# Kernel optimization log

Hardware: AMD Instinct MI355X
Metric: run time of the kernel (lower is better)

The kernel has to match this reference:

```python
import jax, jax.numpy as jnp
import numpy as np

B, D_MODEL, C, T = 2, 256, 64, 1024
N_HEADS = 8
EPS = 1e-5


def setup_inputs() -> dict:
    key = jax.random.key(0)
    k1, k2, k3 = jax.random.split(key, 3)
    x = jax.random.normal(k1, (B, D_MODEL, C, T), dtype=jnp.float32)
    in_w = jax.random.normal(k2, (3 * D_MODEL, D_MODEL), dtype=jnp.float32) * 0.05
    in_b = jnp.zeros((3 * D_MODEL,), jnp.float32)
    out_w = jax.random.normal(k3, (D_MODEL, D_MODEL), dtype=jnp.float32) * 0.05
    out_b = jnp.zeros((D_MODEL,), jnp.float32)
    return dict(x=x, in_w=in_w, in_b=in_b, out_w=out_w, out_b=out_b)


def reference(x, in_w, in_b, out_w, out_b):
    b, d, c, t = x.shape
    h = N_HEADS
    f = d // h
    scale = 1.0 / np.sqrt(f).astype(np.float32)

    # InstanceNorm2d (no affine): normalize each (b, channel) over spatial (c, t)
    mu = x.mean(axis=(2, 3), keepdims=True)
    var = x.var(axis=(2, 3), keepdims=True)  # biased, as torch
    xn = (x - mu) / jnp.sqrt(var + EPS)

    # 1x1 conv d -> 3d
    qkv = jnp.einsum('bdct,ed->bect', xn, in_w) + in_b[None, :, None, None]
    q, k, v = jnp.split(qkv, 3, axis=1)

    def to_heads(u):
        # b (h f) c t -> (b c) h f t
        u = u.reshape(b, h, f, c, t)
        u = u.transpose(0, 3, 1, 2, 4)
        return u.reshape(b * c, h, f, t)

    q = jax.nn.softmax(to_heads(q), axis=-2) * scale  # softmax over feature dim
    k = jax.nn.softmax(to_heads(k), axis=-1)          # softmax over length dim
    v = to_heads(v) / t

    # context: [n, h, f_k, f_v]
    ctx = jnp.einsum('nhkl,nhvl->nhkv', k, v)
    out = jnp.einsum('nhdv,nhdl->nhvl', ctx, q)

    # (b c) h f t -> b (h f) c t
    out = out.reshape(b, c, h, f, t).transpose(0, 2, 3, 1, 4).reshape(b, d, c, t)

    out = jnp.einsum('bdct,ed->bect', out, out_w) + out_b[None, :, None, None]
    return out + x
```

## Files before the change

kernel.cpp:

```cpp
#include <hip/hip_runtime.h>
#include <stdint.h>

#define D_MODEL 256
#define TDIM    1024
#define NHEADS  8
#define FDIM    32
#define P_LEN   65536
#define K3      768
#define BK      64

using u16 = unsigned short;

typedef __bf16 bf16x8 __attribute__((ext_vector_type(8)));
typedef float  floatx4 __attribute__((ext_vector_type(4)));

__device__ __forceinline__ float b2f(u16 u) {
    union { float f; uint32_t i; } v; v.i = ((uint32_t)u) << 16; return v.f;
}
__device__ __forceinline__ u16 f2b(float f) {
    union { float f; uint32_t i; } v; v.f = f;
    uint32_t i = v.i;
    uint32_t r = i + 0x7fffu + ((i >> 16) & 1u);
    return (u16)(r >> 16);
}

__device__ __forceinline__ void gload_lds16(const u16* g, u16* l) {
    __builtin_amdgcn_global_load_lds((const __attribute__((address_space(1))) void*)g,
                                     (__attribute__((address_space(3))) void*)l,
                                     16, 0, 0);
}

__device__ __forceinline__ void stc(u16* p, float v) { *p = f2b(v); }
__device__ __forceinline__ void stc(float* p, float v) { *p = v; }

__global__ __launch_bounds__(256) void stats_kernel(const float* __restrict__ x,
                                                    float* __restrict__ mu,
                                                    float* __restrict__ rstd) {
    int bd = blockIdx.x;
    const float* row = x + (size_t)bd * P_LEN;
    int tid = threadIdx.x;
    float s = 0.f, sq = 0.f;
    for (int i = 0; i < P_LEN / (256 * 4); ++i) {
        int idx = (i * 256 + tid) * 4;
        float4 u = *(const float4*)(row + idx);
        s += u.x + u.y + u.z + u.w;
        sq += u.x * u.x + u.y * u.y + u.z * u.z + u.w * u.w;
    }
    for (int off = 32; off; off >>= 1) { s += __shfl_down(s, off); sq += __shfl_down(sq, off); }
    __shared__ float rs[4], rq[4];
    if ((tid & 63) == 0) { rs[tid >> 6] = s; rq[tid >> 6] = sq; }
    __syncthreads();
    if (tid == 0) {
        float S = rs[0] + rs[1] + rs[2] + rs[3];
        float Q = rq[0] + rq[1] + rq[2] + rq[3];
        float m = S * (1.f / 65536.f);
        float var = Q * (1.f / 65536.f) - m * m;
        mu[bd] = m;
        rstd[bd] = rsqrtf(var + 1e-5f);
    }
}

__global__ __launch_bounds__(256) void fold_kernel(const float* __restrict__ in_w,
                                                   const float* __restrict__ in_b,
                                                   const float* __restrict__ mu,
                                                   const float* __restrict__ rstd,
                                                   u16* __restrict__ Wp,
                                                   float* __restrict__ bprime) {
    int bid = blockIdx.x;
    int b = bid / K3, e = bid % K3;
    int d = threadIdx.x;
    float w = in_w[e * D_MODEL + d];
    float r = rstd[b * D_MODEL + d];
    float m = mu[b * D_MODEL + d];
    Wp[(size_t)bid * D_MODEL + d] = f2b(w * r);
    float contrib = w * r * m;
    for (int off = 32; off; off >>= 1) contrib += __shfl_down(contrib, off);
    __shared__ float rr[4];
    if ((d & 63) == 0) rr[d >> 6] = contrib;
    __syncthreads();
    if (d == 0) bprime[bid] = in_b[e] - (rr[0] + rr[1] + rr[2] + rr[3]);
}

__global__ void cvt_w(const float* __restrict__ w, u16* __restrict__ o) {
    int i = blockIdx.x * 256 + threadIdx.x;
    o[i] = f2b(w[i]);
}

__global__ __launch_bounds__(256) void transpose_x(const float* __restrict__ x,
                                                   u16* __restrict__ xt) {
    __shared__ float tile[64][65];
    int p0 = blockIdx.x * 64;
    int d0 = blockIdx.y * 64;
    int tid = threadIdx.x;
    int dr = tid >> 4;
    int pc = (tid & 15) * 4;
#pragma unroll
    for (int it = 0; it < 4; ++it) {
        int d = it * 16 + dr;
        float4 v = *(const float4*)&x[(size_t)(d0 + d) * P_LEN + p0 + pc];
        tile[pc + 0][d] = v.x;
        tile[pc + 1][d] = v.y;
        tile[pc + 2][d] = v.z;
        tile[pc + 3][d] = v.w;
    }
    __syncthreads();
    int pr = tid >> 3;
    int dc = (tid & 7) * 8;
#pragma unroll
    for (int it = 0; it < 2; ++it) {
        int p = it * 32 + pr;
        ushort4 o0 = make_ushort4(f2b(tile[p][dc + 0]), f2b(tile[p][dc + 1]),
                                  f2b(tile[p][dc + 2]), f2b(tile[p][dc + 3]));
        ushort4 o1 = make_ushort4(f2b(tile[p][dc + 4]), f2b(tile[p][dc + 5]),
                                  f2b(tile[p][dc + 6]), f2b(tile[p][dc + 7]));
        u16* dst = xt + (size_t)(p0 + p) * D_MODEL + d0 + dc;
        *(ushort4*)dst = o0;
        *(ushort4*)(dst + 4) = o1;
    }
}

template <bool RESID, typename OT>
__global__ __launch_bounds__(256) void mgemm(const u16* __restrict__ A,
                                             const u16* __restrict__ Bt,
                                             const float* __restrict__ bias,
                                             const float* __restrict__ resid,
                                             OT* __restrict__ Cout) {
    __shared__ __align__(16) u16 As[128 * BK];
    __shared__ __align__(16) u16 Bs[128 * BK];
    const int tid  = threadIdx.x;
    const int wave = tid >> 6;
    const int lane = tid & 63;
    const int m0 = blockIdx.y * 128;
    const int p0 = blockIdx.x * 128;
    const int mw = (wave >> 1) * 64;
    const int nw = (wave & 1) * 64;

    floatx4 acc[4][4];
#pragma unroll
    for (int i = 0; i < 4; ++i)
#pragma unroll
        for (int j = 0; j < 4; ++j) acc[i][j] = (floatx4){0.f, 0.f, 0.f, 0.f};

    const int srow = lane >> 3;
    const int schunk = lane & 7;
    const int q  = lane >> 4;
    const int rl = lane & 15;

    for (int s = 0; s < 4; ++s) {
        const int k0 = s * BK;
#pragma unroll
        for (int j = 0; j < 4; ++j) {
            int rbase = wave * 32 + j * 8;
            int r = rbase + srow;
            int cg = schunk ^ (r & 7);
            gload_lds16(A  + ((size_t)(m0 + r) << 8) + k0 + cg * 8, &As[rbase * BK]);
            gload_lds16(Bt + ((size_t)(p0 + r) << 8) + k0 + cg * 8, &Bs[rbase * BK]);
        }
        __syncthreads();
#pragma unroll
        for (int ks = 0; ks < 2; ++ks) {
            bf16x8 af[4], bf[4];
#pragma unroll
            for (int ti = 0; ti < 4; ++ti) {
                int r = mw + 16 * ti + rl;
                int cp = (ks * 4 + q) ^ (r & 7);
                af[ti] = *(const bf16x8*)&As[r * BK + cp * 8];
            }
#pragma unroll
            for (int tj = 0; tj < 4; ++tj) {
                int r = nw + 16 * tj + rl;
                int cp = (ks * 4 + q) ^ (r & 7);
                bf[tj] = *(const bf16x8*)&Bs[r * BK + cp * 8];
            }
#pragma unroll
            for (int ti = 0; ti < 4; ++ti)
#pragma unroll
                for (int tj = 0; tj < 4; ++tj)
                    acc[ti][tj] = __builtin_amdgcn_mfma_f32_16x16x32_bf16(
                        af[ti], bf[tj], acc[ti][tj], 0, 0, 0);
        }
        __syncthreads();
    }

#pragma unroll
    for (int ti = 0; ti < 4; ++ti) {
#pragma unroll
        for (int i = 0; i < 4; ++i) {
            int e = m0 + mw + 16 * ti + 4 * q + i;
            float bv = bias[e];
            size_t rowbase = (size_t)e * P_LEN + p0 + nw;
#pragma unroll
            for (int tj = 0; tj < 4; ++tj) {
                size_t addr = rowbase + 16 * tj + rl;
                float v = acc[ti][tj][i] + bv;
                if (RESID) v += resid[addr];
                stc(Cout + addr, v);
            }
        }
    }
}

__global__ __launch_bounds__(256) void attn_k(const u16* __restrict__ qkv,
                                              u16* __restrict__ attT) {
    int bid = blockIdx.x;
    int c = bid >> 3, h = bid & 7;
    int tid = threadIdx.x;
    size_t colbase = (size_t)c * TDIM;
    const u16* qb = qkv + (size_t)(h * FDIM) * P_LEN + colbase;
    const u16* kb = qkv + (size_t)(D_MODEL + h * FDIM) * P_LEN + colbase;
    const u16* vb = qkv + (size_t)(2 * D_MODEL + h * FDIM) * P_LEN + colbase;

    __shared__ float kmax[32], kinv[32];
    __shared__ float ekt[32][65];
    __shared__ float vt[64][36];
    __shared__ float ctxs[32][36];

    int row = tid >> 3, g = tid & 7;
    const u16* krow = kb + (size_t)row * P_LEN;

    float m = -1e30f;
    for (int i = 0; i < 32; ++i) {
        ushort4 u = *(const ushort4*)(krow + g * 4 + i * 32);
        m = fmaxf(m, fmaxf(fmaxf(b2f(u.x), b2f(u.y)), fmaxf(b2f(u.z), b2f(u.w))));
    }
    for (int off = 4; off; off >>= 1) m = fmaxf(m, __shfl_down(m, off, 8));
    if (g == 0) kmax[row] = m;
    __syncthreads();
    float rm = kmax[row];
    float s = 0.f;
    for (int i = 0; i < 32; ++i) {
        ushort4 u = *(const ushort4*)(krow + g * 4 + i * 32);
        s += __expf(b2f(u.x) - rm) + __expf(b2f(u.y) - rm) +
             __expf(b2f(u.z) - rm) + __expf(b2f(u.w) - rm);
    }
    for (int off = 4; off; off >>= 1) s += __shfl_down(s, off, 8);
    if (g == 0) kinv[row] = 1.f / (s * (float)TDIM);
    __syncthreads();

    float mymax = kmax[row];
    float myinv = kinv[row];
    const u16* vrow = vb + (size_t)row * P_LEN;

    int kd = tid >> 3, vg = tid & 7;
    float cacc[4] = {0.f, 0.f, 0.f, 0.f};
    for (int tile = 0; tile < 16; ++tile) {
        int t0 = tile * 64;
        int col = g * 8;
        ushort4 u1 = *(const ushort4*)(krow + t0 + col);
        ushort4 u2 = *(const ushort4*)(krow + t0 + col + 4);
        ushort4 w1 = *(const ushort4*)(vrow + t0 + col);
        ushort4 w2 = *(const ushort4*)(vrow + t0 + col + 4);
        __syncthreads();
        ekt[row][col + 0] = __expf(b2f(u1.x) - mymax) * myinv;
        ekt[row][col + 1] = __expf(b2f(u1.y) - mymax) * myinv;
        ekt[row][col + 2] = __expf(b2f(u1.z) - mymax) * myinv;
        ekt[row][col + 3] = __expf(b2f(u1.w) - mymax) * myinv;
        ekt[row][col + 4] = __expf(b2f(u2.x) - mymax) * myinv;
        ekt[row][col + 5] = __expf(b2f(u2.y) - mymax) * myinv;
        ekt[row][col + 6] = __expf(b2f(u2.z) - mymax) * myinv;
        ekt[row][col + 7] = __expf(b2f(u2.w) - mymax) * myinv;
        vt[col + 0][row] = b2f(w1.x);
        vt[col + 1][row] = b2f(w1.y);
        vt[col + 2][row] = b2f(w1.z);
        vt[col + 3][row] = b2f(w1.w);
        vt[col + 4][row] = b2f(w2.x);
        vt[col + 5][row] = b2f(w2.y);
        vt[col + 6][row] = b2f(w2.z);
        vt[col + 7][row] = b2f(w2.w);
        __syncthreads();
#pragma unroll 16
        for (int t = 0; t < 64; ++t) {
            float e = ekt[kd][t];
            float4 v4 = *(const float4*)&vt[t][vg * 4];
            cacc[0] += e * v4.x;
            cacc[1] += e * v4.y;
            cacc[2] += e * v4.z;
            cacc[3] += e * v4.w;
        }
    }
    __syncthreads();
    const float scale = 0.17677669529663687f;
    ctxs[kd][vg * 4 + 0] = cacc[0] * scale;
    ctxs[kd][vg * 4 + 1] = cacc[1] * scale;
    ctxs[kd][vg * 4 + 2] = cacc[2] * scale;
    ctxs[kd][vg * 4 + 3] = cacc[3] * scale;
    __syncthreads();

    for (int pair = 0; pair < 2; ++pair) {
        int t1 = tid + pair * 512;
        int t2 = t1 + 256;
        float pa[32], pb[32];
        float ma = -1e30f, mb = -1e30f;
#pragma unroll
        for (int f = 0; f < 32; ++f) {
            pa[f] = b2f(qb[(size_t)f * P_LEN + t1]);
            pb[f] = b2f(qb[(size_t)f * P_LEN + t2]);
            ma = fmaxf(ma, pa[f]);
            mb = fmaxf(mb, pb[f]);
        }
        float sa = 0.f, sb = 0.f;
#pragma unroll
        for (int f = 0; f < 32; ++f) {
            pa[f] = __expf(pa[f] - ma); sa += pa[f];
            pb[f] = __expf(pb[f] - mb); sb += pb[f];
        }
        float ia = 1.f / sa, ib = 1.f / sb;
#pragma unroll
        for (int f = 0; f < 32; ++f) { pa[f] *= ia; pb[f] *= ib; }

        size_t r1 = (size_t)(colbase + t1) * D_MODEL + h * FDIM;
        size_t r2 = (size_t)(colbase + t2) * D_MODEL + h * FDIM;
        for (int vg2 = 0; vg2 < 8; ++vg2) {
            float4 a1 = {0.f, 0.f, 0.f, 0.f}, a2 = {0.f, 0.f, 0.f, 0.f};
#pragma unroll
            for (int kd2 = 0; kd2 < 32; ++kd2) {
                float4 c4 = *(const float4*)&ctxs[kd2][vg2 * 4];
                a1.x += pa[kd2] * c4.x; a1.y += pa[kd2] * c4.y;
                a1.z += pa[kd2] * c4.z; a1.w += pa[kd2] * c4.w;
                a2.x += pb[kd2] * c4.x; a2.y += pb[kd2] * c4.y;
                a2.z += pb[kd2] * c4.z; a2.w += pb[kd2] * c4.w;
            }
            *(ushort4*)&attT[r1 + vg2 * 4] =
                make_ushort4(f2b(a1.x), f2b(a1.y), f2b(a1.z), f2b(a1.w));
            *(ushort4*)&attT[r2 + vg2 * 4] =
                make_ushort4(f2b(a2.x), f2b(a2.y), f2b(a2.z), f2b(a2.w));
        }
    }
}

extern "C" void kernel_launch(void* const* d_in, const int* in_sizes, int n_in,
                              void* d_out, int out_size, void* d_ws, size_t ws_size,
                              hipStream_t stream) {
    const float* x     = (const float*)d_in[0];
    const float* in_w  = (const float*)d_in[1];
    const float* in_b  = (const float*)d_in[2];
    const float* out_w = (const float*)d_in[3];
    const float* out_b = (const float*)d_in[4];
    float* out = (float*)d_out;

    char* ws = (char*)d_ws;
    float* mu     = (float*)(ws);
    float* rstd   = (float*)(ws + 2048);
    u16*   Wp     = (u16*)(ws + 4096);
    float* bprime = (float*)(ws + 790528);
    u16*   Wp2    = (u16*)(ws + 796672);
    u16*   tbuf   = (u16*)(ws + 927744);
    u16*   qkvb   = (u16*)(ws + 34482176);

    stats_kernel<<<512, 256, 0, stream>>>(x, mu, rstd);
    fold_kernel<<<1536, 256, 0, stream>>>(in_w, in_b, mu, rstd, Wp, bprime);
    cvt_w<<<256, 256, 0, stream>>>(out_w, Wp2);

    for (int b = 0; b < 2; ++b) {
        const float* xb = x + (size_t)b * D_MODEL * P_LEN;
        transpose_x<<<dim3(1024, 4), 256, 0, stream>>>(xb, tbuf);
        mgemm<false, u16><<<dim3(512, 6), 256, 0, stream>>>(
            Wp + (size_t)b * K3 * D_MODEL, tbuf, bprime + b * K3, nullptr, qkvb);
        attn_k<<<512, 256, 0, stream>>>(qkvb, tbuf);
        mgemm<true, float><<<dim3(512, 2), 256, 0, stream>>>(
            Wp2, tbuf, out_b, xb, out + (size_t)b * D_MODEL * P_LEN);
    }
}
```

Baseline: 642.5 us.

## Fold attention context into per-channel output weights and use MFMA for context

Splits the attention kernel in two. One kernel computes the q softmax and writes it in transposed layout. The other computes the k-softmax·vᵀ context with bf16 MFMA on LDS tiles. A new wfold kernel multiplies out_w by each per-c context, producing per-channel folded weights. The output GEMM then reads its A operand per channel block, so the context multiply is absorbed into that GEMM and the scalar per-token context product disappears. The max subtraction in both softmaxes is dropped, which risks exp overflow for large activations. The ctx and folded-weight buffers reuse the q region of the qkv buffer after it has been consumed.

```diff
diff --git a/kernel.cpp b/kernel.cpp
--- a/kernel.cpp
+++ b/kernel.cpp
@@ -17,11 +17,20 @@
 __device__ __forceinline__ float b2f(u16 u) {
     union { float f; uint32_t i; } v; v.i = ((uint32_t)u) << 16; return v.f;
 }
+__device__ __forceinline__ float b2f_lo(uint32_t u) {
+    union { float f; uint32_t i; } v; v.i = u << 16; return v.f;
+}
+__device__ __forceinline__ float b2f_hi(uint32_t u) {
+    union { float f; uint32_t i; } v; v.i = u & 0xffff0000u; return v.f;
+}
 __device__ __forceinline__ u16 f2b(float f) {
     union { float f; uint32_t i; } v; v.f = f;
     uint32_t i = v.i;
     uint32_t r = i + 0x7fffu + ((i >> 16) & 1u);
     return (u16)(r >> 16);
+}
+__device__ __forceinline__ uint32_t pack2(float lo, float hi) {
+    return ((uint32_t)f2b(hi) << 16) | (uint32_t)f2b(lo);
 }
 
 __device__ __forceinline__ void gload_lds16(const u16* g, u16* l) {
@@ -81,11 +90,6 @@
     if (d == 0) bprime[bid] = in_b[e] - (rr[0] + rr[1] + rr[2] + rr[3]);
 }
 
-__global__ void cvt_w(const float* __restrict__ w, u16* __restrict__ o) {
-    int i = blockIdx.x * 256 + threadIdx.x;
-    o[i] = f2b(w[i]);
-}
-
 __global__ __launch_bounds__(256) void transpose_x(const float* __restrict__ x,
                                                    u16* __restrict__ xt) {
     __shared__ float tile[64][65];
@@ -119,7 +123,7 @@
     }
 }
 
-template <bool RESID, typename OT>
+template <bool RESID, bool PERC, typename OT>
 __global__ __launch_bounds__(256) void mgemm(const u16* __restrict__ A,
                                              const u16* __restrict__ Bt,
                                              const float* __restrict__ bias,
@@ -135,6 +139,8 @@
     const int mw = (wave >> 1) * 64;
     const int nw = (wave & 1) * 64;
 
+    const u16* Ab = PERC ? A + ((size_t)(blockIdx.x >> 3) << 16) : A;
+
     floatx4 acc[4][4];
 #pragma unroll
     for (int i = 0; i < 4; ++i)
@@ -153,7 +159,7 @@
             int rbase = wave * 32 + j * 8;
             int r = rbase + srow;
             int cg = schunk ^ (r & 7);
-            gload_lds16(A  + ((size_t)(m0 + r) << 8) + k0 + cg * 8, &As[rbase * BK]);
+            gload_lds16(Ab + ((size_t)(m0 + r) << 8) + k0 + cg * 8, &As[rbase * BK]);
             gload_lds16(Bt + ((size_t)(p0 + r) << 8) + k0 + cg * 8, &Bs[rbase * BK]);
         }
         __syncthreads();
@@ -200,130 +206,156 @@
     }
 }
 
-__global__ __launch_bounds__(256) void attn_k(const u16* __restrict__ qkv,
-                                              u16* __restrict__ attT) {
+__global__ __launch_bounds__(256) void qsm_kernel(const u16* __restrict__ qkv,
+                                                  u16* __restrict__ pq) {
+    int tid = threadIdx.x;
+    int pair = tid >> 2;
+    int hq = tid & 3;
+    size_t p = (size_t)blockIdx.x * 128 + (size_t)pair * 2;
+    const u16* qb = qkv + p;
+#pragma unroll
+    for (int hi = 0; hi < 2; ++hi) {
+        int h = hq * 2 + hi;
+        const u16* qh = qb + (size_t)(h * FDIM) * P_LEN;
+        float a[32], b[32];
+#pragma unroll
+        for (int f = 0; f < 32; ++f) {
+            uint32_t uu = *(const uint32_t*)(qh + (size_t)f * P_LEN);
+            a[f] = __expf(b2f_lo(uu));
+            b[f] = __expf(b2f_hi(uu));
+        }
+        float sa = 0.f, sb = 0.f;
+#pragma unroll
+        for (int f = 0; f < 32; ++f) { sa += a[f]; sb += b[f]; }
+        sa = 1.f / sa; sb = 1.f / sb;
+        u16* o1 = pq + p * D_MODEL + h * FDIM;
+        u16* o2 = o1 + D_MODEL;
+#pragma unroll
+        for (int c = 0; c < 4; ++c) {
+            union { u16 u[8]; uint4 v4; } pka, pkb;
+#pragma unroll
+            for (int i = 0; i < 8; ++i) {
+                pka.u[i] = f2b(a[c * 8 + i] * sa);
+                pkb.u[i] = f2b(b[c * 8 + i] * sb);
+            }
+            *(uint4*)(o1 + c * 8) = pka.v4;
+            *(uint4*)(o2 + c * 8) = pkb.v4;
+        }
+    }
+}
+
+__global__ __launch_bounds__(256) void ctx_kernel(const u16* __restrict__ qkv,
+                                                  float* __restrict__ ctx) {
     int bid = blockIdx.x;
     int c = bid >> 3, h = bid & 7;
     int tid = threadIdx.x;
     size_t colbase = (size_t)c * TDIM;
-    const u16* qb = qkv + (size_t)(h * FDIM) * P_LEN + colbase;
     const u16* kb = qkv + (size_t)(D_MODEL + h * FDIM) * P_LEN + colbase;
     const u16* vb = qkv + (size_t)(2 * D_MODEL + h * FDIM) * P_LEN + colbase;
 
-    __shared__ float kmax[32], kinv[32];
-    __shared__ float ekt[32][65];
-    __shared__ float vt[64][36];
-    __shared__ float ctxs[32][36];
-
-    int row = tid >> 3, g = tid & 7;
-    const u16* krow = kb + (size_t)row * P_LEN;
-
-    float m = -1e30f;
-    for (int i = 0; i < 32; ++i) {
-        ushort4 u = *(const ushort4*)(krow + g * 4 + i * 32);
-        m = fmaxf(m, fmaxf(fmaxf(b2f(u.x), b2f(u.y)), fmaxf(b2f(u.z), b2f(u.w))));
-    }
-    for (int off = 4; off; off >>= 1) m = fmaxf(m, __shfl_down(m, off, 8));
-    if (g == 0) kmax[row] = m;
-    __syncthreads();
-    float rm = kmax[row];
-    float s = 0.f;
-    for (int i = 0; i < 32; ++i) {
-        ushort4 u = *(const ushort4*)(krow + g * 4 + i * 32);
-        s += __expf(b2f(u.x) - rm) + __expf(b2f(u.y) - rm) +
-             __expf(b2f(u.z) - rm) + __expf(b2f(u.w) - rm);
-    }
-    for (int off = 4; off; off >>= 1) s += __shfl_down(s, off, 8);
-    if (g == 0) kinv[row] = 1.f / (s * (float)TDIM);
-    __syncthreads();
-
-    float mymax = kmax[row];
-    float myinv = kinv[row];
-    const u16* vrow = vb + (size_t)row * P_LEN;
-
-    int kd = tid >> 3, vg = tid & 7;
-    float cacc[4] = {0.f, 0.f, 0.f, 0.f};
-    for (int tile = 0; tile < 16; ++tile) {
-        int t0 = tile * 64;
-        int col = g * 8;
-        ushort4 u1 = *(const ushort4*)(krow + t0 + col);
-        ushort4 u2 = *(const ushort4*)(krow + t0 + col + 4);
-        ushort4 w1 = *(const ushort4*)(vrow + t0 + col);
-        ushort4 w2 = *(const ushort4*)(vrow + t0 + col + 4);
+    __shared__ float kinv[32];
+    __shared__ __align__(16) u16 ekt[32 * 264];
+    __shared__ __align__(16) u16 vsb[32 * 264];
+
+    {
+        int row = tid >> 3, g = tid & 7;
+        const u16* krow = kb + (size_t)row * P_LEN;
+        float s = 0.f;
+#pragma unroll
+        for (int i = 0; i < 16; ++i) {
+            uint4 u = *(const uint4*)(krow + g * 8 + i * 64);
+            s += __expf(b2f_lo(u.x)) + __expf(b2f_hi(u.x))
+               + __expf(b2f_lo(u.y)) + __expf(b2f_hi(u.y))
+               + __expf(b2f_lo(u.z)) + __expf(b2f_hi(u.z))
+               + __expf(b2f_lo(u.w)) + __expf(b2f_hi(u.w));
+        }
+        for (int off = 4; off; off >>= 1) s += __shfl_down(s, off, 8);
+        if (g == 0) kinv[row] = 0.17677669529663687f / (s * 1024.f);
+    }
+    __syncthreads();
+
+    const int lane = tid & 63;
+    const int wave = tid >> 6;
+    const int rl = lane & 15, q = lane >> 4;
+    const int mi = wave >> 1, ni = wave & 1;
+    const int o  = tid & 31;
+    const int r8 = tid >> 5;
+    floatx4 acc = {0.f, 0.f, 0.f, 0.f};
+
+    for (int ch = 0; ch < 4; ++ch) {
+        int t0 = ch * 256;
+        if (ch) __syncthreads();
+#pragma unroll
+        for (int pass = 0; pass < 4; ++pass) {
+            int r = pass * 8 + r8;
+            float iv = kinv[r];
+            uint4 u = *((const uint4*)(kb + (size_t)r * P_LEN + t0) + o);
+            uint4 w = *((const uint4*)(vb + (size_t)r * P_LEN + t0) + o);
+            uint4 E;
+            E.x = pack2(__expf(b2f_lo(u.x)) * iv, __expf(b2f_hi(u.x)) * iv);
+            E.y = pack2(__expf(b2f_lo(u.y)) * iv, __expf(b2f_hi(u.y)) * iv);
+            E.z = pack2(__expf(b2f_lo(u.z)) * iv, __expf(b2f_hi(u.z)) * iv);
+            E.w = pack2(__expf(b2f_lo(u.w)) * iv, __expf(b2f_hi(u.w)) * iv);
+            *(uint4*)&ekt[r * 264 + o * 8] = E;
+            *(uint4*)&vsb[r * 264 + o * 8] = w;
+        }
         __syncthreads();
-        ekt[row][col + 0] = __expf(b2f(u1.x) - mymax) * myinv;
-        ekt[row][col + 1] = __expf(b2f(u1.y) - mymax) * myinv;
-        ekt[row][col + 2] = __expf(b2f(u1.z) - mymax) * myinv;
-        ekt[row][col + 3] = __expf(b2f(u1.w) - mymax) * myinv;
-        ekt[row][col + 4] = __expf(b2f(u2.x) - mymax) * myinv;
-        ekt[row][col + 5] = __expf(b2f(u2.y) - mymax) * myinv;
-        ekt[row][col + 6] = __expf(b2f(u2.z) - mymax) * myinv;
-        ekt[row][col + 7] = __expf(b2f(u2.w) - mymax) * myinv;
-        vt[col + 0][row] = b2f(w1.x);
-        vt[col + 1][row] = b2f(w1.y);
-        vt[col + 2][row] = b2f(w1.z);
-        vt[col + 3][row] = b2f(w1.w);
-        vt[col + 4][row] = b2f(w2.x);
-        vt[col + 5][row] = b2f(w2.y);
-        vt[col + 6][row] = b2f(w2.z);
-        vt[col + 7][row] = b2f(w2.w);
-        __syncthreads();
-#pragma unroll 16
-        for (int t = 0; t < 64; ++t) {
-            float e = ekt[kd][t];
-            float4 v4 = *(const float4*)&vt[t][vg * 4];
-            cacc[0] += e * v4.x;
-            cacc[1] += e * v4.y;
-            cacc[2] += e * v4.z;
-            cacc[3] += e * v4.w;
-        }
-    }
-    __syncthreads();
-    const float scale = 0.17677669529663687f;
-    ctxs[kd][vg * 4 + 0] = cacc[0] * scale;
-    ctxs[kd][vg * 4 + 1] = cacc[1] * scale;
-    ctxs[kd][vg * 4 + 2] = cacc[2] * scale;
-    ctxs[kd][vg * 4 + 3] = cacc[3] * scale;
-    __syncthreads();
-
-    for (int pair = 0; pair < 2; ++pair) {
-        int t1 = tid + pair * 512;
-        int t2 = t1 + 256;
-        float pa[32], pb[32];
-        float ma = -1e30f, mb = -1e30f;
-#pragma unroll
-        for (int f = 0; f < 32; ++f) {
-            pa[f] = b2f(qb[(size_t)f * P_LEN + t1]);
-            pb[f] = b2f(qb[(size_t)f * P_LEN + t2]);
-            ma = fmaxf(ma, pa[f]);
-            mb = fmaxf(mb, pb[f]);
-        }
-        float sa = 0.f, sb = 0.f;
-#pragma unroll
-        for (int f = 0; f < 32; ++f) {
-            pa[f] = __expf(pa[f] - ma); sa += pa[f];
-            pb[f] = __expf(pb[f] - mb); sb += pb[f];
-        }
-        float ia = 1.f / sa, ib = 1.f / sb;
-#pragma unroll
-        for (int f = 0; f < 32; ++f) { pa[f] *= ia; pb[f] *= ib; }
-
-        size_t r1 = (size_t)(colbase + t1) * D_MODEL + h * FDIM;
-        size_t r2 = (size_t)(colbase + t2) * D_MODEL + h * FDIM;
-        for (int vg2 = 0; vg2 < 8; ++vg2) {
-            float4 a1 = {0.f, 0.f, 0.f, 0.f}, a2 = {0.f, 0.f, 0.f, 0.f};
-#pragma unroll
-            for (int kd2 = 0; kd2 < 32; ++kd2) {
-                float4 c4 = *(const float4*)&ctxs[kd2][vg2 * 4];
-                a1.x += pa[kd2] * c4.x; a1.y += pa[kd2] * c4.y;
-                a1.z += pa[kd2] * c4.z; a1.w += pa[kd2] * c4.w;
-                a2.x += pb[kd2] * c4.x; a2.y += pb[kd2] * c4.y;
-                a2.z += pb[kd2] * c4.z; a2.w += pb[kd2] * c4.w;
-            }
-            *(ushort4*)&attT[r1 + vg2 * 4] =
-                make_ushort4(f2b(a1.x), f2b(a1.y), f2b(a1.z), f2b(a1.w));
-            *(ushort4*)&attT[r2 + vg2 * 4] =
-                make_ushort4(f2b(a2.x), f2b(a2.y), f2b(a2.z), f2b(a2.w));
+#pragma unroll
+        for (int ks = 0; ks < 8; ++ks) {
+            bf16x8 a  = *(const bf16x8*)&ekt[(16 * mi + rl) * 264 + ks * 32 + q * 8];
+            bf16x8 bv = *(const bf16x8*)&vsb[(16 * ni + rl) * 264 + ks * 32 + q * 8];
+            acc = __builtin_amdgcn_mfma_f32_16x16x32_bf16(a, bv, acc, 0, 0, 0);
+        }
+    }
+
+    float* co = ctx + (size_t)bid * 1024;
+#pragma unroll
+    for (int i = 0; i < 4; ++i)
+        co[(16 * mi + 4 * q + i) * 32 + 16 * ni + rl] = acc[i];
+}
+
+__global__ __launch_bounds__(256) void wfold_kernel(const float* __restrict__ w2,
+                                                    const float* __restrict__ ctx,
+                                                    u16* __restrict__ w2p) {
+    __shared__ float cs[8192];
+    int c = blockIdx.x;
+    int tid = threadIdx.x;
+    const float4* cb = (const float4*)(ctx + (size_t)c * 8192);
+#pragma unroll
+    for (int i = 0; i < 8; ++i)
+        ((float4*)cs)[i * 256 + tid] = cb[i * 256 + tid];
+    __syncthreads();
+    int e = blockIdx.y * 128 + (tid >> 1);
+    int hh = tid & 1;
+    const float* wrow = w2 + (size_t)e * 256;
+    u16* orow = w2p + ((size_t)c << 16) + (size_t)e * 256;
+#pragma unroll
+    for (int hi = 0; hi < 4; ++hi) {
+        int h = hh * 4 + hi;
+        float w[32];
+#pragma unroll
+        for (int v = 0; v < 8; ++v) {
+            float4 t4 = *(const float4*)&wrow[h * 32 + v * 4];
+            w[v * 4 + 0] = t4.x; w[v * 4 + 1] = t4.y;
+            w[v * 4 + 2] = t4.z; w[v * 4 + 3] = t4.w;
+        }
+        const float* chp = cs + h * 1024;
+#pragma unroll
+        for (int kc = 0; kc < 4; ++kc) {
+            union { u16 u[8]; uint4 v4; } pk;
+#pragma unroll
+            for (int ki = 0; ki < 8; ++ki) {
+                const float* ck = chp + (kc * 8 + ki) * 32;
+                float acc = 0.f;
+#pragma unroll
+                for (int v = 0; v < 32; v += 4) {
+                    float4 c4 = *(const float4*)&ck[v];
+                    acc += w[v] * c4.x + w[v + 1] * c4.y
+                         + w[v + 2] * c4.z + w[v + 3] * c4.w;
+                }
+                pk.u[ki] = f2b(acc);
+            }
+            *(uint4*)(orow + h * 32 + kc * 8) = pk.v4;
         }
     }
 }
@@ -343,21 +375,23 @@
     float* rstd   = (float*)(ws + 2048);
     u16*   Wp     = (u16*)(ws + 4096);
     float* bprime = (float*)(ws + 790528);
-    u16*   Wp2    = (u16*)(ws + 796672);
-    u16*   tbuf   = (u16*)(ws + 927744);
-    u16*   qkvb   = (u16*)(ws + 34482176);
+    u16*   tbuf   = (u16*)(ws + 796672);
+    u16*   qkvb   = (u16*)(ws + 34351104);
+    float* ctxb   = (float*)(ws + 34351104);
+    u16*   w2p    = (u16*)(ws + 34351104 + 4194304);
 
     stats_kernel<<<512, 256, 0, stream>>>(x, mu, rstd);
     fold_kernel<<<1536, 256, 0, stream>>>(in_w, in_b, mu, rstd, Wp, bprime);
-    cvt_w<<<256, 256, 0, stream>>>(out_w, Wp2);
 
     for (int b = 0; b < 2; ++b) {
         const float* xb = x + (size_t)b * D_MODEL * P_LEN;
         transpose_x<<<dim3(1024, 4), 256, 0, stream>>>(xb, tbuf);
-        mgemm<false, u16><<<dim3(512, 6), 256, 0, stream>>>(
+        mgemm<false, false, u16><<<dim3(512, 6), 256, 0, stream>>>(
             Wp + (size_t)b * K3 * D_MODEL, tbuf, bprime + b * K3, nullptr, qkvb);
-        attn_k<<<512, 256, 0, stream>>>(qkvb, tbuf);
-        mgemm<true, float><<<dim3(512, 2), 256, 0, stream>>>(
-            Wp2, tbuf, out_b, xb, out + (size_t)b * D_MODEL * P_LEN);
-    }
-}
+        qsm_kernel<<<512, 256, 0, stream>>>(qkvb, tbuf);
+        ctx_kernel<<<512, 256, 0, stream>>>(qkvb, ctxb);
+        wfold_kernel<<<dim3(64, 2), 256, 0, stream>>>(out_w, ctxb, w2p);
+        mgemm<true, true, float><<<dim3(512, 2), 256, 0, stream>>>(
+            w2p, tbuf, out_b, xb, out + (size_t)b * D_MODEL * P_LEN);
+    }
+}
```

After: 611.8 us. -4.8%, faster.
